# Optimization experiments

Hardware: AMD Instinct MI355X
Metric: run time of the kernel (lower is better)

Reference implementation:

```python
import jax, jax.numpy as jnp
import numpy as np

KH, KW = 3, 3
PAD, STRIDE, DIL, GROUPS = 1, 1, 1, 1
KK = KH * KW


def setup_inputs() -> dict:
    key = jax.random.key(0)
    ks = jax.random.split(key, 5)
    B, Cin, H, W = 8, 256, 64, 64
    Cout = 256
    x = jax.random.normal(ks[0], (B, Cin, H, W), jnp.float32)
    # offset conv: Conv2d(Cin -> 2*KK, 3x3, pad 1), small init so offsets are modest
    w_off = jax.random.normal(ks[1], (2 * KK, Cin, KH, KW), jnp.float32) * 0.01
    b_off = jax.random.normal(ks[2], (2 * KK,), jnp.float32) * 0.01
    # deformable conv weights: [Cout, Cin/groups, KH, KW]
    w_dcn = jax.random.normal(ks[3], (Cout, Cin // GROUPS, KH, KW), jnp.float32) * 0.05
    b_dcn = jax.random.normal(ks[4], (Cout,), jnp.float32) * 0.05
    return {"x": x, "w_off": w_off, "b_off": b_off, "w_dcn": w_dcn, "b_dcn": b_dcn}


def _deform_conv2d(x, offsets, w, b):
    """Deformable conv v1 (torchvision semantics, zero padding outside image).
    x: [B,Cin,Hin,Win], offsets: [B,2*KK,Ho,Wo] with (dy,dx) interleaved per tap.
    """
    B, Cin, Hin, Win = x.shape
    Ho, Wo = offsets.shape[2], offsets.shape[3]
    Cout = w.shape[0]

    off = offsets.reshape(B, KK, 2, Ho, Wo)
    off_y, off_x = off[:, :, 0], off[:, :, 1]  # [B,KK,Ho,Wo]

    # base sampling grid per kernel tap k = kh*KW + kw
    base_ky = (jnp.repeat(jnp.arange(KH), KW) * DIL).astype(jnp.float32)  # [KK]
    base_kx = (jnp.tile(jnp.arange(KW), KH) * DIL).astype(jnp.float32)
    hs = (jnp.arange(Ho) * STRIDE - PAD).astype(jnp.float32)
    ws = (jnp.arange(Wo) * STRIDE - PAD).astype(jnp.float32)

    py = hs[None, None, :, None] + base_ky[None, :, None, None] + off_y  # [B,KK,Ho,Wo]
    px = ws[None, None, None, :] + base_kx[None, :, None, None] + off_x

    iy0f = jnp.floor(py)
    ix0f = jnp.floor(px)
    fy = py - iy0f
    fx = px - ix0f
    iy0 = iy0f.astype(jnp.int32)
    ix0 = ix0f.astype(jnp.int32)

    x_flat = x.reshape(B, Cin, Hin * Win)

    def gather(iy, ix, wgt):
        valid = (iy >= 0) & (iy < Hin) & (ix >= 0) & (ix < Win)
        idx = (jnp.clip(iy, 0, Hin - 1) * Win + jnp.clip(ix, 0, Win - 1)).reshape(B, -1)
        vals = jnp.take_along_axis(x_flat, idx[:, None, :], axis=2)  # [B,Cin,KK*Ho*Wo]
        return vals * (wgt * valid).reshape(B, 1, -1)

    samp = (gather(iy0, ix0, (1 - fy) * (1 - fx))
            + gather(iy0, ix0 + 1, (1 - fy) * fx)
            + gather(iy0 + 1, ix0, fy * (1 - fx))
            + gather(iy0 + 1, ix0 + 1, fy * fx))  # [B,Cin,KK*Ho*Wo]

    samp = samp.reshape(B, GROUPS, Cin // GROUPS, KK, Ho, Wo)
    wg = w.reshape(GROUPS, Cout // GROUPS, Cin // GROUPS, KK)
    out = jnp.einsum('gock,bgckhw->bgohw', wg, samp).reshape(B, Cout, Ho, Wo)
    return out + b[None, :, None, None]


def reference(x, w_off, b_off, w_dcn, b_dcn):
    offsets = jax.lax.conv_general_dilated(
        x, w_off, window_strides=(STRIDE, STRIDE),
        padding=[(PAD, PAD), (PAD, PAD)], rhs_dilation=(DIL, DIL),
        dimension_numbers=('NCHW', 'OIHW', 'NCHW')) + b_off[None, :, None, None]
    return _deform_conv2d(x, offsets, w_dcn, b_dcn)
```

## Files before the change

kernel.cpp:

```cpp
#include <hip/hip_runtime.h>

#define HN 64
#define WN 64
#define HW 4096
#define CIN 256
#define COUT 256
#define NKK 9
#define OFFC 18
#define KTOT 2304
#define CICH 32
#define KCH 288
#define SROW 296
#define NCHUNK 8

typedef __attribute__((ext_vector_type(8))) short bf16x8;
typedef __attribute__((ext_vector_type(4))) float f32x4;

static __device__ __forceinline__ unsigned short f2bf(float f) {
    unsigned u = __float_as_uint(f);
    return (unsigned short)((u + 0x7FFFu + ((u >> 16) & 1u)) >> 16);
}
static __device__ __forceinline__ unsigned pk2(float a, float b) {
    return (unsigned)f2bf(a) | ((unsigned)f2bf(b) << 16);
}
static __device__ __forceinline__ float bf2f(short s) {
    return __uint_as_float(((unsigned)(unsigned short)s) << 16);
}

__global__ __launch_bounds__(256) void prep_kernel(
    const float* __restrict__ x, const float* __restrict__ w_dcn,
    const float* __restrict__ w_off, unsigned short* __restrict__ xh,
    unsigned short* __restrict__ wd_b, unsigned short* __restrict__ wo_b)
{
    const int blk = blockIdx.x;
    const int t = threadIdx.x;
    if (blk < 512) {
        __shared__ unsigned short lds[64 * 264];
        const int b = blk >> 6;
        const int row = blk & 63;
        const int p = t & 63;
        const int cb = (t >> 6) * 8;
        const float* xp = x + (size_t)b * CIN * HW + row * WN + p;
#pragma unroll
        for (int i = 0; i < 8; ++i) {
            const int c0 = cb + i * 32;
            float v[8];
#pragma unroll
            for (int j = 0; j < 8; ++j)
                v[j] = xp[(size_t)(c0 + j) * HW];
            uint4 o = { pk2(v[0],v[1]), pk2(v[2],v[3]), pk2(v[4],v[5]), pk2(v[6],v[7]) };
            *(uint4*)&lds[p * 264 + c0] = o;
        }
        __syncthreads();
        unsigned short* op = xh + ((size_t)b * HW + row * WN) * CIN;
#pragma unroll
        for (int i = 0; i < 8; ++i) {
            const int idx = i * 256 + t;
            const int cg = idx & 31, pp = idx >> 5;
            *(uint4*)(op + (size_t)pp * CIN + cg * 8) = *(const uint4*)&lds[pp * 264 + cg * 8];
        }
    } else if (blk < 768) {
        const int cout = blk - 512;
        for (int id = t; id < 288; id += 256) {
            const int k = id * 8;
            const int kk = k >> 8, c0 = k & 255;
            const float* wp = w_dcn + (size_t)cout * KTOT + kk;
            float v[8];
#pragma unroll
            for (int j = 0; j < 8; ++j) v[j] = wp[(size_t)(c0 + j) * NKK];
            uint4 o = { pk2(v[0],v[1]), pk2(v[2],v[3]), pk2(v[4],v[5]), pk2(v[6],v[7]) };
            *(uint4*)(wd_b + (size_t)cout * KTOT + k) = o;
        }
    } else {
        const int r = blk - 768;
        for (int id = t; id < 288; id += 256) {
            const int k = id * 8;
            const int kk = k >> 8, c0 = k & 255;
            uint4 o = {0u, 0u, 0u, 0u};
            if (r < OFFC) {
                const float* wp = w_off + (size_t)r * KTOT + kk;
                float v[8];
#pragma unroll
                for (int j = 0; j < 8; ++j) v[j] = wp[(size_t)(c0 + j) * NKK];
                o = (uint4){ pk2(v[0],v[1]), pk2(v[2],v[3]), pk2(v[4],v[5]), pk2(v[6],v[7]) };
            }
            *(uint4*)(wo_b + (size_t)r * KTOT + k) = o;
        }
    }
}

__global__ __launch_bounds__(256) void offs_mfma_kernel(
    const unsigned short* __restrict__ xh, const unsigned short* __restrict__ wo_b,
    const float* __restrict__ b_off, float* __restrict__ offs)
{
    const int blk = blockIdx.x;
    const int b = blk & 7;
    const int tile = blk >> 3;
    const int ty0 = (tile >> 3) << 3;
    const int tx0 = (tile & 7) << 3;
    const int t = threadIdx.x;
    const int lane = t & 63;
    const int wave = t >> 6;
    const int pxl = wave * 16 + (lane & 15);
    const int kq8 = (lane >> 4) * 8;
    const int oy = ty0 + (pxl >> 3);
    const int ox = tx0 + (pxl & 7);
    const unsigned short* xb = xh + (size_t)b * HW * CIN + kq8;
    const unsigned short* wrow = wo_b + (size_t)(lane & 15) * KTOT + kq8;

    f32x4 acc0 = {0.f,0.f,0.f,0.f}, acc1 = {0.f,0.f,0.f,0.f};
#pragma unroll
    for (int kk = 0; kk < 9; ++kk) {
        const int yy = oy + kk / 3 - 1;
        const int xx = ox + kk % 3 - 1;
        const bool valid = ((unsigned)yy < HN) && ((unsigned)xx < WN);
        const unsigned short* bp = xb + (size_t)(yy * WN + xx) * CIN;
        const unsigned short* wp = wrow + kk * 256;
#pragma unroll
        for (int s = 0; s < 8; ++s) {
            const bf16x8 bfr = valid ? *(const bf16x8*)(bp + s * 32)
                                     : (bf16x8){0,0,0,0,0,0,0,0};
            const bf16x8 a0 = *(const bf16x8*)(wp + s * 32);
            const bf16x8 a1 = *(const bf16x8*)(wp + (size_t)16 * KTOT + s * 32);
            acc0 = __builtin_amdgcn_mfma_f32_16x16x32_bf16(a0, bfr, acc0, 0, 0, 0);
            acc1 = __builtin_amdgcn_mfma_f32_16x16x32_bf16(a1, bfr, acc1, 0, 0, 0);
        }
    }
    const int wy = ty0 + (pxl >> 3), wx = tx0 + (pxl & 7);
#pragma unroll
    for (int j = 0; j < 4; ++j) {
        const int c0 = (lane >> 4) * 4 + j;
        if (c0 < OFFC)
            offs[((size_t)b * OFFC + c0) * HW + wy * WN + wx] = acc0[j] + b_off[c0];
        const int c1 = 16 + c0;
        if (c1 < OFFC)
            offs[((size_t)b * OFFC + c1) * HW + wy * WN + wx] = acc1[j] + b_off[c1];
    }
}

static __device__ __forceinline__ void sample_one(
    int id, const unsigned short* __restrict__ xb, int ci0,
    const uint4* __restrict__ tidx, const float4* __restrict__ twgt,
    unsigned short* __restrict__ samp)
{
    const int kk = id >> 8;
    const int px = (id >> 2) & 63;
    const int g  = id & 3;
    const uint4  ti = tidx[kk * 64 + px];
    const float4 tw = twgt[kk * 64 + px];
    const unsigned short* base = xb + ci0 + g * 8;
    const bf16x8 A  = *(const bf16x8*)(base + ti.x);
    const bf16x8 Bv = *(const bf16x8*)(base + ti.y);
    float v[8];
#pragma unroll
    for (int e = 0; e < 8; ++e) v[e] = tw.x * bf2f(A[e]) + tw.y * bf2f(Bv[e]);
    const bf16x8 Cv = *(const bf16x8*)(base + ti.z);
    const bf16x8 Dv = *(const bf16x8*)(base + ti.w);
#pragma unroll
    for (int e = 0; e < 8; ++e) v[e] += tw.z * bf2f(Cv[e]) + tw.w * bf2f(Dv[e]);
    uint4 o = { pk2(v[0],v[1]), pk2(v[2],v[3]), pk2(v[4],v[5]), pk2(v[6],v[7]) };
    *(uint4*)&samp[px * SROW + kk * 32 + g * 8] = o;
}

__global__ __launch_bounds__(1024, 8) void dcn_mfma_kernel(
    const unsigned short* __restrict__ xh, const float* __restrict__ offs,
    const unsigned short* __restrict__ wd_b, const float* __restrict__ bias,
    float* __restrict__ out)
{
    __shared__ unsigned short samp[64 * SROW];
    __shared__ uint4  tidx[576];
    __shared__ float4 twgt[576];

    const int blk = blockIdx.x;
    const int b = blk & 7;
    const int tile = blk >> 3;
    const int ty0 = (tile >> 3) << 3;
    const int tx0 = (tile & 7) << 3;
    const int t = threadIdx.x;
    const int lane = t & 63;
    const int wave = t >> 6;
    const unsigned short* xb = xh + (size_t)b * HW * CIN;

    for (int i = t; i < 576; i += 1024) {
        const int kk = i >> 6, p = i & 63;
        const int oy = ty0 + (p >> 3), ox = tx0 + (p & 7);
        const float offy = offs[((size_t)b * OFFC + 2 * kk) * HW + oy * WN + ox];
        const float offx = offs[((size_t)b * OFFC + 2 * kk + 1) * HW + oy * WN + ox];
        const int ky = kk / 3;
        const float pyf = (float)(oy - 1 + ky) + offy;
        const float pxf = (float)(ox - 1 + (kk - ky * 3)) + offx;
        const float fy0 = floorf(pyf), fx0 = floorf(pxf);
        const int iy0 = (int)fy0, ix0 = (int)fx0;
        const int iy1 = iy0 + 1, ix1 = ix0 + 1;
        const float fy = pyf - fy0, fx = pxf - fx0;
        const float vy0 = ((unsigned)iy0 < HN) ? 1.f : 0.f;
        const float vy1 = ((unsigned)iy1 < HN) ? 1.f : 0.f;
        const float vx0 = ((unsigned)ix0 < WN) ? 1.f : 0.f;
        const float vx1 = ((unsigned)ix1 < WN) ? 1.f : 0.f;
        const int cy0 = min(max(iy0, 0), HN - 1), cy1 = min(max(iy1, 0), HN - 1);
        const int cx0 = min(max(ix0, 0), WN - 1), cx1 = min(max(ix1, 0), WN - 1);
        tidx[i] = make_uint4((unsigned)(cy0 * WN + cx0) * CIN, (unsigned)(cy0 * WN + cx1) * CIN,
                             (unsigned)(cy1 * WN + cx0) * CIN, (unsigned)(cy1 * WN + cx1) * CIN);
        twgt[i] = make_float4((1.f - fy) * (1.f - fx) * vy0 * vx0,
                              (1.f - fy) * fx * vy0 * vx1,
                              fy * (1.f - fx) * vy1 * vx0,
                              fy * fx * vy1 * vx1);
    }

    f32x4 acc0 = {0.f,0.f,0.f,0.f}, acc1 = {0.f,0.f,0.f,0.f};
    f32x4 acc2 = {0.f,0.f,0.f,0.f}, acc3 = {0.f,0.f,0.f,0.f};

    for (int chunk = 0; chunk < NCHUNK; ++chunk) {
        const int ci0 = chunk * CICH;
        __syncthreads();
        sample_one(t,        xb, ci0, tidx, twgt, samp);
        sample_one(t + 1024, xb, ci0, tidx, twgt, samp);
        if (t < 256) sample_one(t + 2048, xb, ci0, tidx, twgt, samp);
        __syncthreads();
        const unsigned short* wb = wd_b + (size_t)(wave * 16 + (lane & 15)) * KTOT
                                 + ci0 + (lane >> 4) * 8;
        const unsigned short* sb = &samp[(lane & 15) * SROW + (lane >> 4) * 8];
#pragma unroll
        for (int s = 0; s < 9; ++s) {
            const bf16x8 a    = *(const bf16x8*)(wb + s * 256);
            const bf16x8 bfr0 = *(const bf16x8*)(sb + s * 32);
            const bf16x8 bfr1 = *(const bf16x8*)(sb + 16 * SROW + s * 32);
            const bf16x8 bfr2 = *(const bf16x8*)(sb + 32 * SROW + s * 32);
            const bf16x8 bfr3 = *(const bf16x8*)(sb + 48 * SROW + s * 32);
            acc0 = __builtin_amdgcn_mfma_f32_16x16x32_bf16(a, bfr0, acc0, 0, 0, 0);
            acc1 = __builtin_amdgcn_mfma_f32_16x16x32_bf16(a, bfr1, acc1, 0, 0, 0);
            acc2 = __builtin_amdgcn_mfma_f32_16x16x32_bf16(a, bfr2, acc2, 0, 0, 0);
            acc3 = __builtin_amdgcn_mfma_f32_16x16x32_bf16(a, bfr3, acc3, 0, 0, 0);
        }
    }

    const int row4 = (lane >> 4) * 4;
    float bv[4];
#pragma unroll
    for (int j = 0; j < 4; ++j) bv[j] = bias[wave * 16 + row4 + j];
    const f32x4 av[4] = {acc0, acc1, acc2, acc3};
#pragma unroll
    for (int pt = 0; pt < 4; ++pt) {
        const int px = pt * 16 + (lane & 15);
        const int wy = ty0 + (px >> 3), wx = tx0 + (px & 7);
        float* op = out + ((size_t)b * COUT + wave * 16 + row4) * HW + wy * WN + wx;
#pragma unroll
        for (int j = 0; j < 4; ++j)
            op[(size_t)j * HW] = av[pt][j] + bv[j];
    }
}

extern "C" void kernel_launch(void* const* d_in, const int* in_sizes, int n_in,
                              void* d_out, int out_size, void* d_ws, size_t ws_size,
                              hipStream_t stream) {
    const float* x     = (const float*)d_in[0];
    const float* w_off = (const float*)d_in[1];
    const float* b_off = (const float*)d_in[2];
    const float* w_dcn = (const float*)d_in[3];
    const float* b_dcn = (const float*)d_in[4];
    float* out = (float*)d_out;

    float* offs          = (float*)d_ws;
    unsigned short* wd_b = (unsigned short*)((char*)d_ws + 2359296);
    unsigned short* wo_b = (unsigned short*)((char*)d_ws + 2359296 + 1179648);
    unsigned short* xh   = (unsigned short*)((char*)d_ws + 2359296 + 1179648 + 147456);

    prep_kernel<<<800, 256, 0, stream>>>(x, w_dcn, w_off, xh, wd_b, wo_b);
    offs_mfma_kernel<<<512, 256, 0, stream>>>(xh, wo_b, b_off, offs);
    dcn_mfma_kernel<<<512, 1024, 0, stream>>>(xh, offs, wd_b, b_dcn, out);
}
```

Measured before the change: 234.6 us.

## Software-pipeline bilinear gathers for next channel chunk behind MFMA compute

Splits the sampling step into a gather-issue phase and a combine phase. The global loads for the next channel chunk are issued before the MFMA loop of the current chunk, so gather latency overlaps the matrix math. Weight fragments for a whole chunk are loaded into registers ahead of the barrier, and the launch bound's minimum-blocks hint is lowered to allow more registers per thread. The cost is higher register pressure and possibly lower occupancy.

```diff
diff --git a/kernel.cpp b/kernel.cpp
--- a/kernel.cpp
+++ b/kernel.cpp
@@ -138,31 +138,41 @@
     }
 }
 
-static __device__ __forceinline__ void sample_one(
+struct GC { bf16x8 c0, c1, c2, c3; };
+
+static __device__ __forceinline__ void issue_task(
     int id, const unsigned short* __restrict__ xb, int ci0,
-    const uint4* __restrict__ tidx, const float4* __restrict__ twgt,
-    unsigned short* __restrict__ samp)
+    const uint4* __restrict__ tidx, GC& g)
 {
     const int kk = id >> 8;
     const int px = (id >> 2) & 63;
-    const int g  = id & 3;
-    const uint4  ti = tidx[kk * 64 + px];
+    const int gq = id & 3;
+    const uint4 ti = tidx[kk * 64 + px];
+    const unsigned short* base = xb + ci0 + gq * 8;
+    g.c0 = *(const bf16x8*)(base + ti.x);
+    g.c1 = *(const bf16x8*)(base + ti.y);
+    g.c2 = *(const bf16x8*)(base + ti.z);
+    g.c3 = *(const bf16x8*)(base + ti.w);
+}
+
+static __device__ __forceinline__ void combine_task(
+    int id, const float4* __restrict__ twgt, const GC& g,
+    unsigned short* __restrict__ samp)
+{
+    const int kk = id >> 8;
+    const int px = (id >> 2) & 63;
+    const int gq = id & 3;
     const float4 tw = twgt[kk * 64 + px];
-    const unsigned short* base = xb + ci0 + g * 8;
-    const bf16x8 A  = *(const bf16x8*)(base + ti.x);
-    const bf16x8 Bv = *(const bf16x8*)(base + ti.y);
     float v[8];
 #pragma unroll
-    for (int e = 0; e < 8; ++e) v[e] = tw.x * bf2f(A[e]) + tw.y * bf2f(Bv[e]);
-    const bf16x8 Cv = *(const bf16x8*)(base + ti.z);
-    const bf16x8 Dv = *(const bf16x8*)(base + ti.w);
-#pragma unroll
-    for (int e = 0; e < 8; ++e) v[e] += tw.z * bf2f(Cv[e]) + tw.w * bf2f(Dv[e]);
+    for (int e = 0; e < 8; ++e)
+        v[e] = tw.x * bf2f(g.c0[e]) + tw.y * bf2f(g.c1[e])
+             + tw.z * bf2f(g.c2[e]) + tw.w * bf2f(g.c3[e]);
     uint4 o = { pk2(v[0],v[1]), pk2(v[2],v[3]), pk2(v[4],v[5]), pk2(v[6],v[7]) };
-    *(uint4*)&samp[px * SROW + kk * 32 + g * 8] = o;
-}
-
-__global__ __launch_bounds__(1024, 8) void dcn_mfma_kernel(
+    *(uint4*)&samp[px * SROW + kk * 32 + gq * 8] = o;
+}
+
+__global__ __launch_bounds__(1024, 4) void dcn_mfma_kernel(
     const unsigned short* __restrict__ xh, const float* __restrict__ offs,
     const unsigned short* __restrict__ wd_b, const float* __restrict__ bias,
     float* __restrict__ out)
@@ -210,28 +220,44 @@
     f32x4 acc0 = {0.f,0.f,0.f,0.f}, acc1 = {0.f,0.f,0.f,0.f};
     f32x4 acc2 = {0.f,0.f,0.f,0.f}, acc3 = {0.f,0.f,0.f,0.f};
 
+    const unsigned short* wb_base = wd_b + (size_t)(wave * 16 + (lane & 15)) * KTOT
+                                  + (lane >> 4) * 8;
+    const unsigned short* sb = &samp[(lane & 15) * SROW + (lane >> 4) * 8];
+    const bool third = (t < 256);
+
+    __syncthreads();
+    GC g0, g1;
+    issue_task(t,        xb, 0, tidx, g0);
+    issue_task(t + 1024, xb, 0, tidx, g1);
+
     for (int chunk = 0; chunk < NCHUNK; ++chunk) {
         const int ci0 = chunk * CICH;
+        GC g2;
+        if (third) issue_task(t + 2048, xb, ci0, tidx, g2);
+        combine_task(t,        twgt, g0, samp);
+        combine_task(t + 1024, twgt, g1, samp);
+        if (third) combine_task(t + 2048, twgt, g2, samp);
+        bf16x8 a[9];
+#pragma unroll
+        for (int s = 0; s < 9; ++s)
+            a[s] = *(const bf16x8*)(wb_base + ci0 + s * 256);
         __syncthreads();
-        sample_one(t,        xb, ci0, tidx, twgt, samp);
-        sample_one(t + 1024, xb, ci0, tidx, twgt, samp);
-        if (t < 256) sample_one(t + 2048, xb, ci0, tidx, twgt, samp);
-        __syncthreads();
-        const unsigned short* wb = wd_b + (size_t)(wave * 16 + (lane & 15)) * KTOT
-                                 + ci0 + (lane >> 4) * 8;
-        const unsigned short* sb = &samp[(lane & 15) * SROW + (lane >> 4) * 8];
+        if (chunk < NCHUNK - 1) {
+            issue_task(t,        xb, ci0 + CICH, tidx, g0);
+            issue_task(t + 1024, xb, ci0 + CICH, tidx, g1);
+        }
 #pragma unroll
         for (int s = 0; s < 9; ++s) {
-            const bf16x8 a    = *(const bf16x8*)(wb + s * 256);
             const bf16x8 bfr0 = *(const bf16x8*)(sb + s * 32);
             const bf16x8 bfr1 = *(const bf16x8*)(sb + 16 * SROW + s * 32);
             const bf16x8 bfr2 = *(const bf16x8*)(sb + 32 * SROW + s * 32);
             const bf16x8 bfr3 = *(const bf16x8*)(sb + 48 * SROW + s * 32);
-            acc0 = __builtin_amdgcn_mfma_f32_16x16x32_bf16(a, bfr0, acc0, 0, 0, 0);
-            acc1 = __builtin_amdgcn_mfma_f32_16x16x32_bf16(a, bfr1, acc1, 0, 0, 0);
-            acc2 = __builtin_amdgcn_mfma_f32_16x16x32_bf16(a, bfr2, acc2, 0, 0, 0);
-            acc3 = __builtin_amdgcn_mfma_f32_16x16x32_bf16(a, bfr3, acc3, 0, 0, 0);
-        }
+            acc0 = __builtin_amdgcn_mfma_f32_16x16x32_bf16(a[s], bfr0, acc0, 0, 0, 0);
+            acc1 = __builtin_amdgcn_mfma_f32_16x16x32_bf16(a[s], bfr1, acc1, 0, 0, 0);
+            acc2 = __builtin_amdgcn_mfma_f32_16x16x32_bf16(a[s], bfr2, acc2, 0, 0, 0);
+            acc3 = __builtin_amdgcn_mfma_f32_16x16x32_bf16(a[s], bfr3, acc3, 0, 0, 0);
+        }
+        __syncthreads();
     }
 
     const int row4 = (lane >> 4) * 4;
```

Result: slower. 256.6 us (+9.4%).

## Warp-specialize DCN kernel into sampler and MFMA waves with double-buffered LDS

Applied to the files above, without the earlier changes.

Splits the 16 waves of the deformable-conv block so that 12 waves do bilinear sampling of the next channel chunk into a double-buffered LDS tile while 4 waves run the MFMAs on the current one. Each MFMA wave now covers 64 output channels with 16 accumulators, and the sampler issues all 12 gathers before doing any math to raise memory-level parallelism. The goal is to hide gather latency behind the matrix work and to drop one barrier per chunk. In exchange only a quarter of the waves do MFMA, register pressure goes up, LDS use doubles, and the launch-bounds occupancy hint drops from 8 to 2.

```diff
diff --git a/kernel.cpp b/kernel.cpp
--- a/kernel.cpp
+++ b/kernel.cpp
@@ -9,9 +9,9 @@
 #define OFFC 18
 #define KTOT 2304
 #define CICH 32
-#define KCH 288
 #define SROW 296
 #define NCHUNK 8
+#define PROD_T 768
 
 typedef __attribute__((ext_vector_type(8))) short bf16x8;
 typedef __attribute__((ext_vector_type(4))) float f32x4;
@@ -138,36 +138,43 @@
     }
 }
 
-static __device__ __forceinline__ void sample_one(
-    int id, const unsigned short* __restrict__ xb, int ci0,
+static __device__ __forceinline__ void stage3(
+    int t, const unsigned short* __restrict__ xb, int ci0,
     const uint4* __restrict__ tidx, const float4* __restrict__ twgt,
-    unsigned short* __restrict__ samp)
-{
-    const int kk = id >> 8;
-    const int px = (id >> 2) & 63;
-    const int g  = id & 3;
-    const uint4  ti = tidx[kk * 64 + px];
-    const float4 tw = twgt[kk * 64 + px];
-    const unsigned short* base = xb + ci0 + g * 8;
-    const bf16x8 A  = *(const bf16x8*)(base + ti.x);
-    const bf16x8 Bv = *(const bf16x8*)(base + ti.y);
-    float v[8];
-#pragma unroll
-    for (int e = 0; e < 8; ++e) v[e] = tw.x * bf2f(A[e]) + tw.y * bf2f(Bv[e]);
-    const bf16x8 Cv = *(const bf16x8*)(base + ti.z);
-    const bf16x8 Dv = *(const bf16x8*)(base + ti.w);
-#pragma unroll
-    for (int e = 0; e < 8; ++e) v[e] += tw.z * bf2f(Cv[e]) + tw.w * bf2f(Dv[e]);
-    uint4 o = { pk2(v[0],v[1]), pk2(v[2],v[3]), pk2(v[4],v[5]), pk2(v[6],v[7]) };
-    *(uint4*)&samp[px * SROW + kk * 32 + g * 8] = o;
-}
-
-__global__ __launch_bounds__(1024, 8) void dcn_mfma_kernel(
+    unsigned short* __restrict__ buf)
+{
+    int kk[3], px[3], gq[3];
+    bf16x8 c[3][4];
+#pragma unroll
+    for (int r = 0; r < 3; ++r) {
+        const int id = r * PROD_T + t;
+        kk[r] = id >> 8; px[r] = (id >> 2) & 63; gq[r] = id & 3;
+        const uint4 ti = tidx[kk[r] * 64 + px[r]];
+        const unsigned short* base = xb + ci0 + gq[r] * 8;
+        c[r][0] = *(const bf16x8*)(base + ti.x);
+        c[r][1] = *(const bf16x8*)(base + ti.y);
+        c[r][2] = *(const bf16x8*)(base + ti.z);
+        c[r][3] = *(const bf16x8*)(base + ti.w);
+    }
+#pragma unroll
+    for (int r = 0; r < 3; ++r) {
+        const float4 tw = twgt[kk[r] * 64 + px[r]];
+        float v[8];
+#pragma unroll
+        for (int e = 0; e < 8; ++e)
+            v[e] = tw.x * bf2f(c[r][0][e]) + tw.y * bf2f(c[r][1][e])
+                 + tw.z * bf2f(c[r][2][e]) + tw.w * bf2f(c[r][3][e]);
+        uint4 o = { pk2(v[0],v[1]), pk2(v[2],v[3]), pk2(v[4],v[5]), pk2(v[6],v[7]) };
+        *(uint4*)&buf[px[r] * SROW + kk[r] * 32 + gq[r] * 8] = o;
+    }
+}
+
+__global__ __launch_bounds__(1024, 2) void dcn_mfma_kernel(
     const unsigned short* __restrict__ xh, const float* __restrict__ offs,
     const unsigned short* __restrict__ wd_b, const float* __restrict__ bias,
     float* __restrict__ out)
 {
-    __shared__ unsigned short samp[64 * SROW];
+    __shared__ unsigned short samp[2][64 * SROW];
     __shared__ uint4  tidx[576];
     __shared__ float4 twgt[576];
 
@@ -179,6 +186,7 @@
     const int t = threadIdx.x;
     const int lane = t & 63;
     const int wave = t >> 6;
+    const bool producer = (wave < 12);
     const unsigned short* xb = xh + (size_t)b * HW * CIN;
 
     for (int i = t; i < 576; i += 1024) {
@@ -206,47 +214,66 @@
                               fy * (1.f - fx) * vy1 * vx0,
                               fy * fx * vy1 * vx1);
     }
-
-    f32x4 acc0 = {0.f,0.f,0.f,0.f}, acc1 = {0.f,0.f,0.f,0.f};
-    f32x4 acc2 = {0.f,0.f,0.f,0.f}, acc3 = {0.f,0.f,0.f,0.f};
-
-    for (int chunk = 0; chunk < NCHUNK; ++chunk) {
-        const int ci0 = chunk * CICH;
+    __syncthreads();
+
+    if (producer) stage3(t, xb, 0, tidx, twgt, samp[0]);
+    __syncthreads();
+
+    const int cw = wave - 12;
+    f32x4 acc[4][4];
+#pragma unroll
+    for (int i = 0; i < 4; ++i)
+#pragma unroll
+        for (int j = 0; j < 4; ++j) acc[i][j] = (f32x4){0.f, 0.f, 0.f, 0.f};
+
+    const unsigned short* wb0 = wd_b + (size_t)(cw * 64 + (lane & 15)) * KTOT + (lane >> 4) * 8;
+
+    for (int c = 0; c < NCHUNK; ++c) {
+        if (producer) {
+            if (c < NCHUNK - 1)
+                stage3(t, xb, (c + 1) * CICH, tidx, twgt, samp[(c + 1) & 1]);
+        } else {
+            const unsigned short* sbb = &samp[c & 1][(lane & 15) * SROW + (lane >> 4) * 8];
+#pragma unroll
+            for (int ct = 0; ct < 4; ++ct) {
+                const unsigned short* wp = wb0 + (size_t)ct * 16 * KTOT + c * CICH;
+                bf16x8 a[9];
+#pragma unroll
+                for (int s = 0; s < 9; ++s)
+                    a[s] = *(const bf16x8*)(wp + s * 256);
+#pragma unroll
+                for (int s = 0; s < 9; ++s) {
+                    const bf16x8 bfr0 = *(const bf16x8*)(sbb + s * 32);
+                    const bf16x8 bfr1 = *(const bf16x8*)(sbb + 16 * SROW + s * 32);
+                    const bf16x8 bfr2 = *(const bf16x8*)(sbb + 32 * SROW + s * 32);
+                    const bf16x8 bfr3 = *(const bf16x8*)(sbb + 48 * SROW + s * 32);
+                    acc[ct][0] = __builtin_amdgcn_mfma_f32_16x16x32_bf16(a[s], bfr0, acc[ct][0], 0, 0, 0);
+                    acc[ct][1] = __builtin_amdgcn_mfma_f32_16x16x32_bf16(a[s], bfr1, acc[ct][1], 0, 0, 0);
+                    acc[ct][2] = __builtin_amdgcn_mfma_f32_16x16x32_bf16(a[s], bfr2, acc[ct][2], 0, 0, 0);
+                    acc[ct][3] = __builtin_amdgcn_mfma_f32_16x16x32_bf16(a[s], bfr3, acc[ct][3], 0, 0, 0);
+                }
+            }
+        }
         __syncthreads();
-        sample_one(t,        xb, ci0, tidx, twgt, samp);
-        sample_one(t + 1024, xb, ci0, tidx, twgt, samp);
-        if (t < 256) sample_one(t + 2048, xb, ci0, tidx, twgt, samp);
-        __syncthreads();
-        const unsigned short* wb = wd_b + (size_t)(wave * 16 + (lane & 15)) * KTOT
-                                 + ci0 + (lane >> 4) * 8;
-        const unsigned short* sb = &samp[(lane & 15) * SROW + (lane >> 4) * 8];
-#pragma unroll
-        for (int s = 0; s < 9; ++s) {
-            const bf16x8 a    = *(const bf16x8*)(wb + s * 256);
-            const bf16x8 bfr0 = *(const bf16x8*)(sb + s * 32);
-            const bf16x8 bfr1 = *(const bf16x8*)(sb + 16 * SROW + s * 32);
-            const bf16x8 bfr2 = *(const bf16x8*)(sb + 32 * SROW + s * 32);
-            const bf16x8 bfr3 = *(const bf16x8*)(sb + 48 * SROW + s * 32);
-            acc0 = __builtin_amdgcn_mfma_f32_16x16x32_bf16(a, bfr0, acc0, 0, 0, 0);
-            acc1 = __builtin_amdgcn_mfma_f32_16x16x32_bf16(a, bfr1, acc1, 0, 0, 0);
-            acc2 = __builtin_amdgcn_mfma_f32_16x16x32_bf16(a, bfr2, acc2, 0, 0, 0);
-            acc3 = __builtin_amdgcn_mfma_f32_16x16x32_bf16(a, bfr3, acc3, 0, 0, 0);
-        }
-    }
-
-    const int row4 = (lane >> 4) * 4;
-    float bv[4];
-#pragma unroll
-    for (int j = 0; j < 4; ++j) bv[j] = bias[wave * 16 + row4 + j];
-    const f32x4 av[4] = {acc0, acc1, acc2, acc3};
-#pragma unroll
-    for (int pt = 0; pt < 4; ++pt) {
-        const int px = pt * 16 + (lane & 15);
-        const int wy = ty0 + (px >> 3), wx = tx0 + (px & 7);
-        float* op = out + ((size_t)b * COUT + wave * 16 + row4) * HW + wy * WN + wx;
-#pragma unroll
-        for (int j = 0; j < 4; ++j)
-            op[(size_t)j * HW] = av[pt][j] + bv[j];
+    }
+
+    if (!producer) {
+        const int row4 = (lane >> 4) * 4;
+#pragma unroll
+        for (int ct = 0; ct < 4; ++ct) {
+            float bv[4];
+#pragma unroll
+            for (int j = 0; j < 4; ++j) bv[j] = bias[cw * 64 + ct * 16 + row4 + j];
+#pragma unroll
+            for (int pt = 0; pt < 4; ++pt) {
+                const int px = pt * 16 + (lane & 15);
+                const int wy = ty0 + (px >> 3), wx = tx0 + (px & 7);
+                float* op = out + ((size_t)b * COUT + cw * 64 + ct * 16 + row4) * HW + wy * WN + wx;
+#pragma unroll
+                for (int j = 0; j < 4; ++j)
+                    op[(size_t)j * HW] = acc[ct][pt][j] + bv[j];
+            }
+        }
     }
 }
 
```

Result: slower. 312.4 us (+33.2%).

## Double-buffer deformable sampling tile to overlap gather with MFMA compute

Applied to the files above, without the earlier changes.

Turns the single shared sampling buffer into two buffers. The bilinear gather for the next channel chunk now runs while MFMAs consume the current chunk, which drops one barrier per chunk. All global gathers for a chunk are also issued before any blending, to raise memory-level parallelism. In exchange, LDS use roughly doubles (about 75 KB per block), register pressure rises because 12 gathered vectors stay live, and launch bounds fall from 8 to 4 blocks per SM.

```diff
diff --git a/kernel.cpp b/kernel.cpp
--- a/kernel.cpp
+++ b/kernel.cpp
@@ -9,7 +9,6 @@
 #define OFFC 18
 #define KTOT 2304
 #define CICH 32
-#define KCH 288
 #define SROW 296
 #define NCHUNK 8
 
@@ -138,36 +137,12 @@
     }
 }
 
-static __device__ __forceinline__ void sample_one(
-    int id, const unsigned short* __restrict__ xb, int ci0,
-    const uint4* __restrict__ tidx, const float4* __restrict__ twgt,
-    unsigned short* __restrict__ samp)
-{
-    const int kk = id >> 8;
-    const int px = (id >> 2) & 63;
-    const int g  = id & 3;
-    const uint4  ti = tidx[kk * 64 + px];
-    const float4 tw = twgt[kk * 64 + px];
-    const unsigned short* base = xb + ci0 + g * 8;
-    const bf16x8 A  = *(const bf16x8*)(base + ti.x);
-    const bf16x8 Bv = *(const bf16x8*)(base + ti.y);
-    float v[8];
-#pragma unroll
-    for (int e = 0; e < 8; ++e) v[e] = tw.x * bf2f(A[e]) + tw.y * bf2f(Bv[e]);
-    const bf16x8 Cv = *(const bf16x8*)(base + ti.z);
-    const bf16x8 Dv = *(const bf16x8*)(base + ti.w);
-#pragma unroll
-    for (int e = 0; e < 8; ++e) v[e] += tw.z * bf2f(Cv[e]) + tw.w * bf2f(Dv[e]);
-    uint4 o = { pk2(v[0],v[1]), pk2(v[2],v[3]), pk2(v[4],v[5]), pk2(v[6],v[7]) };
-    *(uint4*)&samp[px * SROW + kk * 32 + g * 8] = o;
-}
-
-__global__ __launch_bounds__(1024, 8) void dcn_mfma_kernel(
+__global__ __launch_bounds__(1024, 4) void dcn_mfma_kernel(
     const unsigned short* __restrict__ xh, const float* __restrict__ offs,
     const unsigned short* __restrict__ wd_b, const float* __restrict__ bias,
     float* __restrict__ out)
 {
-    __shared__ unsigned short samp[64 * SROW];
+    __shared__ unsigned short samp[2][64 * SROW];
     __shared__ uint4  tidx[576];
     __shared__ float4 twgt[576];
 
@@ -180,6 +155,7 @@
     const int lane = t & 63;
     const int wave = t >> 6;
     const unsigned short* xb = xh + (size_t)b * HW * CIN;
+    const bool third = (t < 256);
 
     for (int i = t; i < 576; i += 1024) {
         const int kk = i >> 6, p = i & 63;
@@ -206,32 +182,94 @@
                               fy * (1.f - fx) * vy1 * vx0,
                               fy * fx * vy1 * vx1);
     }
+    __syncthreads();
+
+    {
+        bf16x8 g[3][4];
+#pragma unroll
+        for (int r = 0; r < 3; ++r) {
+            if (r == 2 && !third) break;
+            const int id = r * 1024 + t;
+            const uint4 ti = tidx[(id >> 8) * 64 + ((id >> 2) & 63)];
+            const unsigned short* base = xb + (id & 3) * 8;
+            g[r][0] = *(const bf16x8*)(base + ti.x);
+            g[r][1] = *(const bf16x8*)(base + ti.y);
+            g[r][2] = *(const bf16x8*)(base + ti.z);
+            g[r][3] = *(const bf16x8*)(base + ti.w);
+        }
+#pragma unroll
+        for (int r = 0; r < 3; ++r) {
+            if (r == 2 && !third) break;
+            const int id = r * 1024 + t;
+            const int kk = id >> 8, px = (id >> 2) & 63, gq = id & 3;
+            const float4 tw = twgt[kk * 64 + px];
+            float v[8];
+#pragma unroll
+            for (int e = 0; e < 8; ++e)
+                v[e] = tw.x * bf2f(g[r][0][e]) + tw.y * bf2f(g[r][1][e])
+                     + tw.z * bf2f(g[r][2][e]) + tw.w * bf2f(g[r][3][e]);
+            uint4 o = { pk2(v[0],v[1]), pk2(v[2],v[3]), pk2(v[4],v[5]), pk2(v[6],v[7]) };
+            *(uint4*)&samp[0][px * SROW + kk * 32 + gq * 8] = o;
+        }
+    }
+    __syncthreads();
 
     f32x4 acc0 = {0.f,0.f,0.f,0.f}, acc1 = {0.f,0.f,0.f,0.f};
     f32x4 acc2 = {0.f,0.f,0.f,0.f}, acc3 = {0.f,0.f,0.f,0.f};
 
-    for (int chunk = 0; chunk < NCHUNK; ++chunk) {
-        const int ci0 = chunk * CICH;
-        __syncthreads();
-        sample_one(t,        xb, ci0, tidx, twgt, samp);
-        sample_one(t + 1024, xb, ci0, tidx, twgt, samp);
-        if (t < 256) sample_one(t + 2048, xb, ci0, tidx, twgt, samp);
-        __syncthreads();
-        const unsigned short* wb = wd_b + (size_t)(wave * 16 + (lane & 15)) * KTOT
-                                 + ci0 + (lane >> 4) * 8;
-        const unsigned short* sb = &samp[(lane & 15) * SROW + (lane >> 4) * 8];
+    const unsigned short* wb_base = wd_b + (size_t)(wave * 16 + (lane & 15)) * KTOT
+                                  + (lane >> 4) * 8;
+    const unsigned short* sb_base = (lane & 15) * SROW + (lane >> 4) * 8
+                                  + (const unsigned short*)nullptr - (const unsigned short*)nullptr
+                                  + (const unsigned short*)samp[0];
+    (void)sb_base;
+
+    for (int c = 0; c < NCHUNK; ++c) {
+        const int cur = c & 1;
+        if (c < NCHUNK - 1) {
+            const int ci1 = (c + 1) * CICH;
+            bf16x8 g[3][4];
+#pragma unroll
+            for (int r = 0; r < 3; ++r) {
+                if (r == 2 && !third) break;
+                const int id = r * 1024 + t;
+                const uint4 ti = tidx[(id >> 8) * 64 + ((id >> 2) & 63)];
+                const unsigned short* base = xb + ci1 + (id & 3) * 8;
+                g[r][0] = *(const bf16x8*)(base + ti.x);
+                g[r][1] = *(const bf16x8*)(base + ti.y);
+                g[r][2] = *(const bf16x8*)(base + ti.z);
+                g[r][3] = *(const bf16x8*)(base + ti.w);
+            }
+#pragma unroll
+            for (int r = 0; r < 3; ++r) {
+                if (r == 2 && !third) break;
+                const int id = r * 1024 + t;
+                const int kk = id >> 8, px = (id >> 2) & 63, gq = id & 3;
+                const float4 tw = twgt[kk * 64 + px];
+                float v[8];
+#pragma unroll
+                for (int e = 0; e < 8; ++e)
+                    v[e] = tw.x * bf2f(g[r][0][e]) + tw.y * bf2f(g[r][1][e])
+                         + tw.z * bf2f(g[r][2][e]) + tw.w * bf2f(g[r][3][e]);
+                uint4 o = { pk2(v[0],v[1]), pk2(v[2],v[3]), pk2(v[4],v[5]), pk2(v[6],v[7]) };
+                *(uint4*)&samp[cur ^ 1][px * SROW + kk * 32 + gq * 8] = o;
+            }
+        }
+        const unsigned short* sbb = &samp[cur][(lane & 15) * SROW + (lane >> 4) * 8];
+        const unsigned short* wp = wb_base + c * CICH;
 #pragma unroll
         for (int s = 0; s < 9; ++s) {
-            const bf16x8 a    = *(const bf16x8*)(wb + s * 256);
-            const bf16x8 bfr0 = *(const bf16x8*)(sb + s * 32);
-            const bf16x8 bfr1 = *(const bf16x8*)(sb + 16 * SROW + s * 32);
-            const bf16x8 bfr2 = *(const bf16x8*)(sb + 32 * SROW + s * 32);
-            const bf16x8 bfr3 = *(const bf16x8*)(sb + 48 * SROW + s * 32);
+            const bf16x8 a    = *(const bf16x8*)(wp + s * 256);
+            const bf16x8 bfr0 = *(const bf16x8*)(sbb + s * 32);
+            const bf16x8 bfr1 = *(const bf16x8*)(sbb + 16 * SROW + s * 32);
+            const bf16x8 bfr2 = *(const bf16x8*)(sbb + 32 * SROW + s * 32);
+            const bf16x8 bfr3 = *(const bf16x8*)(sbb + 48 * SROW + s * 32);
             acc0 = __builtin_amdgcn_mfma_f32_16x16x32_bf16(a, bfr0, acc0, 0, 0, 0);
             acc1 = __builtin_amdgcn_mfma_f32_16x16x32_bf16(a, bfr1, acc1, 0, 0, 0);
             acc2 = __builtin_amdgcn_mfma_f32_16x16x32_bf16(a, bfr2, acc2, 0, 0, 0);
             acc3 = __builtin_amdgcn_mfma_f32_16x16x32_bf16(a, bfr3, acc3, 0, 0, 0);
         }
+        __syncthreads();
     }
 
     const int row4 = (lane >> 4) * 4;
```

After: 232.4 us. Within noise of the previous version (-0.9%).
